# Kernel tuning notes

Hardware: AMD Instinct MI355X
Metric: run time of the kernel (lower is better)

## Reference

```python
import jax, jax.numpy as jnp
import numpy as np


def setup_inputs() -> dict:
    key = jax.random.key(0)
    k1, k2 = jax.random.split(key)
    B, C, KX, KZ = 512, 256, 6, 22
    x = jax.random.normal(k1, (B, C, KX, KX), dtype=jnp.float32)  # exemplar (kernel)
    z = jax.random.normal(k2, (B, C, KZ, KZ), dtype=jnp.float32)  # search region (input)
    return {"x": x, "z": z}


def reference(x, z):
    # Per-sample cross-correlation: out[b] = conv2d(z[b], x[b]) (valid, stride 1).
    # Expressed as a single grouped convolution with groups=B instead of a
    # Python loop of B separate conv2d calls.
    B, C, kz, _ = z.shape
    z2 = z.reshape(1, B * C, kz, kz)              # [1, B*C, kz, kz]
    out = jax.lax.conv_general_dilated(
        z2, x,
        window_strides=(1, 1),
        padding="VALID",
        dimension_numbers=("NCHW", "OIHW", "NCHW"),
        feature_group_count=B,
    )                                              # [1, B, ho, wo]
    return jnp.transpose(out, (1, 0, 2, 3))        # [B, 1, ho, wo]
```

## Files before the change

### kernel.cpp

```cpp
#include <hip/hip_runtime.h>
#include <cstdint>
#include <cstddef>

#define BB      512
#define CC      256
#define KXX     6
#define KZZ     22
#define HO      17
#define OUTHW   (HO * HO)
#define ZCH     (KZZ * KZZ)
#define XCH     (KXX * KXX)

#define CHUNK_C   8
#define NCHUNK    (CC / CHUNK_C)
#define ZCHUNK    (CHUNK_C * ZCH)
#define XCHUNK    (CHUNK_C * XCH)
#define NT        320
#define NW        5

typedef const __attribute__((address_space(1))) void* gptr_t;
typedef __attribute__((address_space(3))) void* lptr_t;

__device__ __forceinline__ void cp16_async(void* lds_base, const void* gsrc) {
  __builtin_amdgcn_global_load_lds((gptr_t)gsrc, (lptr_t)lds_base, 16, 0, 0);
}
__device__ __forceinline__ void cp4_async(void* lds_base, const void* gsrc) {
  __builtin_amdgcn_global_load_lds((gptr_t)gsrc, (lptr_t)lds_base, 4, 0, 0);
}

__device__ __forceinline__ void stage_chunk(float* zdst, float* xdst,
                                            const float* zsrc, const float* xsrc,
                                            int wave, int lane) {
  char* zd = (char*)zdst;
  const char* zs = (const char*)zsrc;
#pragma unroll
  for (int i = 0; i < 3; ++i) {
    const int grp = wave * 3 + i;
    cp16_async(zd + grp * 1024, zs + grp * 1024 + lane * 16);
  }
  if (wave == 0) {
    if (lane < 32) cp4_async(zd + 15360, zs + 15360 + lane * 4);
  } else if (wave == 1) {
    cp16_async((char*)xdst, (const char*)xsrc + lane * 16);
  } else if (wave == 2) {
    if (lane < 32) cp4_async((char*)xdst + 1024, (const char*)xsrc + 1024 + lane * 4);
  }
}

__global__ __launch_bounds__(NT, 2) void corr_kernel(const float* __restrict__ x,
                                                     const float* __restrict__ z,
                                                     float* __restrict__ out) {
  __shared__ __align__(16) float zbuf[2][ZCHUNK];
  __shared__ __align__(16) float xbuf[2][XCHUNK];

  const int b    = blockIdx.x;
  const int t    = threadIdx.x;
  const int wave = t >> 6;
  const int lane = t & 63;

  const float* zb = z + (size_t)b * (CC * ZCH);
  const float* xb = x + (size_t)b * (CC * XCH);

  stage_chunk(zbuf[0], xbuf[0], zb, xb, wave, lane);

  const int  g      = t / 17;
  const int  oy     = t - g * 17;
  const int  cl     = g & 7;
  const int  kyh    = g >> 3;
  const bool active = (g < 16);

  float acc[HO];
#pragma unroll
  for (int i = 0; i < HO; ++i) acc[i] = 0.0f;

  for (int k = 0; k < NCHUNK; ++k) {
    const int buf = k & 1;
    __syncthreads();

    if (k + 1 < NCHUNK)
      stage_chunk(zbuf[buf ^ 1], xbuf[buf ^ 1],
                  zb + (size_t)(k + 1) * ZCHUNK, xb + (size_t)(k + 1) * XCHUNK,
                  wave, lane);

    if (active) {
      const float* zc = &zbuf[buf][cl * ZCH];
      const float* xc = &xbuf[buf][cl * XCH + kyh * (3 * KXX)];

      __align__(16) float xv[3 * KXX];
#pragma unroll
      for (int i = 0; i < 9; ++i)
        ((float2*)xv)[i] = ((const float2*)xc)[i];

#pragma unroll
      for (int ky2 = 0; ky2 < 3; ++ky2) {
        const int row = oy + kyh * 3 + ky2;
        const float* zr = zc + row * KZZ;
        __align__(16) float zv[KZZ + 1];
#pragma unroll
        for (int i = 0; i < 11; ++i)
          ((float2*)zv)[i] = ((const float2*)zr)[i];
#pragma unroll
        for (int kx = 0; kx < KXX; ++kx) {
          const float xs = xv[ky2 * KXX + kx];
#pragma unroll
          for (int ox = 0; ox < HO; ++ox)
            acc[ox] = fmaf(zv[ox + kx], xs, acc[ox]);
        }
      }
    }
  }

  __syncthreads();
  float* red = &zbuf[0][0];
  if (active) {
#pragma unroll
    for (int ox = 0; ox < HO; ++ox)
      red[g * OUTHW + oy * HO + ox] = acc[ox];
  }
  __syncthreads();
  if (t < OUTHW) {
    float s = 0.0f;
#pragma unroll
    for (int gg = 0; gg < 16; ++gg) s += red[gg * OUTHW + t];
    out[(size_t)b * OUTHW + t] = s;
  }
}

extern "C" void kernel_launch(void* const* d_in, const int* in_sizes, int n_in,
                              void* d_out, int out_size, void* d_ws, size_t ws_size,
                              hipStream_t stream) {
  const float* x = (const float*)d_in[0];
  const float* z = (const float*)d_in[1];
  float* out = (float*)d_out;
  corr_kernel<<<BB, NT, 0, stream>>>(x, z, out);
}
```

Measured before the change: 361.1 us.

## Split channel reduction across four blocks per sample with a second reduce kernel

Each sample's 256 channels are now divided among four blocks, giving 2048 blocks instead of 512. Each block writes its partial 17x17 output to workspace, and a small second kernel sums the four partials. This aims to fill the GPU's many CUs better and raises the launch-bounds occupancy hint from 2 to 4 blocks per CU. The cost is an extra kernel launch, a workspace round-trip, and repeated prologue and epilogue work per block. If the workspace is too small, it falls back to the original single-block-per-sample launch.

New measurement: 368.9 us. 1.02x slower.

```diff
diff --git a/kernel.cpp b/kernel.cpp
--- a/kernel.cpp
+++ b/kernel.cpp
@@ -12,11 +12,10 @@
 #define XCH     (KXX * KXX)
 
 #define CHUNK_C   8
-#define NCHUNK    (CC / CHUNK_C)
 #define ZCHUNK    (CHUNK_C * ZCH)
 #define XCHUNK    (CHUNK_C * XCH)
 #define NT        320
-#define NW        5
+#define SPLITC    4
 
 typedef const __attribute__((address_space(1))) void* gptr_t;
 typedef __attribute__((address_space(3))) void* lptr_t;
@@ -47,19 +46,25 @@
   }
 }
 
-__global__ __launch_bounds__(NT, 2) void corr_kernel(const float* __restrict__ x,
+template <int SPLIT>
+__global__ __launch_bounds__(NT, 4) void corr_kernel(const float* __restrict__ x,
                                                      const float* __restrict__ z,
-                                                     float* __restrict__ out) {
+                                                     float* __restrict__ dst) {
+  constexpr int CPB = CC / SPLIT;
+  constexpr int NCH = CPB / CHUNK_C;
+
   __shared__ __align__(16) float zbuf[2][ZCHUNK];
   __shared__ __align__(16) float xbuf[2][XCHUNK];
 
-  const int b    = blockIdx.x;
+  const int bid  = blockIdx.x;
+  const int b    = bid / SPLIT;
+  const int s    = bid & (SPLIT - 1);
   const int t    = threadIdx.x;
   const int wave = t >> 6;
   const int lane = t & 63;
 
-  const float* zb = z + (size_t)b * (CC * ZCH);
-  const float* xb = x + (size_t)b * (CC * XCH);
+  const float* zb = z + (size_t)b * (CC * ZCH) + (size_t)s * (CPB * ZCH);
+  const float* xb = x + (size_t)b * (CC * XCH) + (size_t)s * (CPB * XCH);
 
   stage_chunk(zbuf[0], xbuf[0], zb, xb, wave, lane);
 
@@ -73,11 +78,11 @@
 #pragma unroll
   for (int i = 0; i < HO; ++i) acc[i] = 0.0f;
 
-  for (int k = 0; k < NCHUNK; ++k) {
+  for (int k = 0; k < NCH; ++k) {
     const int buf = k & 1;
     __syncthreads();
 
-    if (k + 1 < NCHUNK)
+    if (k + 1 < NCH)
       stage_chunk(zbuf[buf ^ 1], xbuf[buf ^ 1],
                   zb + (size_t)(k + 1) * ZCHUNK, xb + (size_t)(k + 1) * XCHUNK,
                   wave, lane);
@@ -119,10 +124,23 @@
   }
   __syncthreads();
   if (t < OUTHW) {
-    float s = 0.0f;
+    float v = 0.0f;
 #pragma unroll
-    for (int gg = 0; gg < 16; ++gg) s += red[gg * OUTHW + t];
-    out[(size_t)b * OUTHW + t] = s;
+    for (int gg = 0; gg < 16; ++gg) v += red[gg * OUTHW + t];
+    dst[(size_t)bid * OUTHW + t] = v;
+  }
+}
+
+__global__ __launch_bounds__(NT) void reduce_kernel(const float* __restrict__ ws,
+                                                    float* __restrict__ out) {
+  const int b = blockIdx.x;
+  const int t = threadIdx.x;
+  if (t < OUTHW) {
+    float v = 0.0f;
+#pragma unroll
+    for (int s = 0; s < SPLITC; ++s)
+      v += ws[(size_t)(b * SPLITC + s) * OUTHW + t];
+    out[(size_t)b * OUTHW + t] = v;
   }
 }
 
@@ -132,5 +150,13 @@
   const float* x = (const float*)d_in[0];
   const float* z = (const float*)d_in[1];
   float* out = (float*)d_out;
-  corr_kernel<<<BB, NT, 0, stream>>>(x, z, out);
+
+  const size_t need = (size_t)BB * SPLITC * OUTHW * sizeof(float);
+  if (ws_size >= need) {
+    float* ws = (float*)d_ws;
+    corr_kernel<SPLITC><<<BB * SPLITC, NT, 0, stream>>>(x, z, ws);
+    reduce_kernel<<<BB, NT, 0, stream>>>(ws, out);
+  } else {
+    corr_kernel<1><<<BB, NT, 0, stream>>>(x, z, out);
+  }
 }
```
